# Performance work log

Measured on AMD Instinct MI355X. Metric: run time of the kernel, lower is better.

Reference implementation:

```python
import jax, jax.numpy as jnp
import numpy as np
import math

HEAD_DIM = 32
N_Q_HEADS = 32
N_KV_HEADS = 8
ROPE_BASE = 10000.0
NEG_INF = -1e9


def _rope_cos_sin(seq_len, dtype):
    inv_freq = 1.0 / (ROPE_BASE ** (jnp.arange(0, HEAD_DIM, 2, dtype=jnp.float32) / HEAD_DIM))
    pos = jnp.arange(seq_len, dtype=jnp.float32)
    freqs = pos[:, None] * inv_freq[None, :]          # [S, D/2]
    emb = jnp.concatenate([freqs, freqs], axis=-1)     # [S, D]
    return jnp.cos(emb).astype(dtype), jnp.sin(emb).astype(dtype)


def _rotate_half(x):
    x1, x2 = jnp.split(x, 2, axis=-1)
    return jnp.concatenate([-x2, x1], axis=-1)


def _apply_rope(x, cos, sin):
    # x: [B, H, S, D]; cos/sin: [S, D]
    return x * cos[None, None] + _rotate_half(x) * sin[None, None]


def setup_inputs() -> dict:
    key = jax.random.key(0)
    ks = jax.random.split(key, 5)
    B, S, D = 2, 2048, 1024
    sc = 1.0 / math.sqrt(D)
    return {
        "hidden_states": jax.random.normal(ks[0], (B, S, D), jnp.float32),
        "attention_mask": jnp.ones((B, S), jnp.int32),
        "Wq": jax.random.normal(ks[1], (1024, 1024), jnp.float32) * sc,
        "Wk": jax.random.normal(ks[2], (256, 1024), jnp.float32) * sc,
        "Wv": jax.random.normal(ks[3], (256, 1024), jnp.float32) * sc,
        "Wo": jax.random.normal(ks[4], (1024, 1024), jnp.float32) * sc,
    }


def reference(hidden_states, attention_mask, Wq, Wk, Wv, Wo):
    B, S, D = hidden_states.shape
    group = N_Q_HEADS // N_KV_HEADS

    q = (hidden_states @ Wq.T).reshape(B, S, N_Q_HEADS, HEAD_DIM).transpose(0, 2, 1, 3)
    k = (hidden_states @ Wk.T).reshape(B, S, N_KV_HEADS, HEAD_DIM).transpose(0, 2, 1, 3)
    v = (hidden_states @ Wv.T).reshape(B, S, N_KV_HEADS, HEAD_DIM).transpose(0, 2, 1, 3)

    cos, sin = _rope_cos_sin(S, q.dtype)
    q = _apply_rope(q, cos, sin)
    k = _apply_rope(k, cos, sin)

    k = jnp.repeat(k, group, axis=1)  # [B, 32, S, D]
    v = jnp.repeat(v, group, axis=1)

    scores = jnp.einsum("bhqd,bhkd->bhqk", q, k) / math.sqrt(HEAD_DIM)

    causal = jnp.tril(jnp.ones((S, S), bool))
    allowed = causal[None, None] & (attention_mask[:, None, None, :] != 0)
    scores = jnp.where(allowed, scores, NEG_INF)

    attn = jax.nn.softmax(scores, axis=-1)
    out = jnp.einsum("bhqk,bhkd->bhqd", attn, v)  # [B, 32, S, 32]
    out = out.transpose(0, 2, 1, 3).reshape(B, S, D)
    return out @ Wo.T
```

## Files before the change

### kernel.cpp

```cpp
#include <hip/hip_runtime.h>

typedef __bf16 bf16x8 __attribute__((ext_vector_type(8)));
typedef __bf16 bf16x4 __attribute__((ext_vector_type(4)));
typedef float f32x4 __attribute__((ext_vector_type(4)));

__device__ __forceinline__ f32x4 mfma16(bf16x8 a, bf16x8 b, f32x4 c) {
  return __builtin_amdgcn_mfma_f32_16x16x32_bf16(a, b, c, 0, 0, 0);
}

__device__ __forceinline__ float fast_exp2(float x) {
  return __builtin_amdgcn_exp2f(x);
}

__global__ __launch_bounds__(256) void prep(const float* __restrict__ hidden,
                                            const float* __restrict__ Wq,
                                            const float* __restrict__ Wk,
                                            const float* __restrict__ Wv,
                                            const float* __restrict__ Wo,
                                            __bf16* __restrict__ hb,
                                            __bf16* __restrict__ Wqkvb,
                                            __bf16* __restrict__ Wob) {
  int q = blockIdx.x * 256 + threadIdx.x;
  const float* src;
  __bf16* dst;
  if (q < 1048576) {
    src = hidden; dst = hb;
  } else if ((q -= 1048576) < 262144) {
    src = Wq; dst = Wqkvb;
  } else if ((q -= 262144) < 65536) {
    src = Wk; dst = Wqkvb + 1048576;
  } else if ((q -= 65536) < 65536) {
    src = Wv; dst = Wqkvb + 1310720;
  } else {
    q -= 65536;
    src = Wo; dst = Wob;
  }
  float4 v = *(const float4*)(src + (size_t)q * 4);
  bf16x4 o = { (__bf16)v.x, (__bf16)v.y, (__bf16)v.z, (__bf16)v.w };
  *(bf16x4*)(dst + (size_t)q * 4) = o;
}

template <bool BF16_OUT>
__global__ __launch_bounds__(256) void gemm_nt(const __bf16* __restrict__ A,
                                               const __bf16* __restrict__ B,
                                               void* __restrict__ Cv, int N) {
  __shared__ __bf16 As[2][128][32];
  __shared__ __bf16 Bs[2][128][32];
  const int m0 = blockIdx.x * 128, n0 = blockIdx.y * 128;
  const int tid = threadIdx.x;
  const int wave = tid >> 6, lane = tid & 63, quad = lane >> 4, l16 = lane & 15;
  const int wr = wave >> 1, wc = wave & 1;
  const int sr = tid >> 1, sc = (tid & 1) * 16;
  f32x4 acc[4][4] = {};
  const __bf16* Ap = A + (size_t)(m0 + sr) * 1024 + sc;
  const __bf16* Bp = B + (size_t)(n0 + sr) * 1024 + sc;
  {
    uint4 a0 = *(const uint4*)Ap, a1 = *(const uint4*)(Ap + 8);
    uint4 b0 = *(const uint4*)Bp, b1 = *(const uint4*)(Bp + 8);
    *(uint4*)&As[0][sr][sc] = a0;
    *(uint4*)&As[0][sr][sc + 8] = a1;
    *(uint4*)&Bs[0][sr][sc] = b0;
    *(uint4*)&Bs[0][sr][sc + 8] = b1;
  }
  __syncthreads();
  int buf = 0;
  for (int k0 = 0; k0 < 1024; k0 += 32) {
    const bool more = (k0 + 32) < 1024;
    uint4 na0, na1, nb0, nb1;
    if (more) {
      na0 = *(const uint4*)(Ap + k0 + 32);
      na1 = *(const uint4*)(Ap + k0 + 40);
      nb0 = *(const uint4*)(Bp + k0 + 32);
      nb1 = *(const uint4*)(Bp + k0 + 40);
    }
    bf16x8 af[4], bfr[4];
#pragma unroll
    for (int i = 0; i < 4; i++)
      af[i] = *(bf16x8*)&As[buf][64 * wr + 16 * i + l16][quad * 8];
#pragma unroll
    for (int j = 0; j < 4; j++)
      bfr[j] = *(bf16x8*)&Bs[buf][64 * wc + 16 * j + l16][quad * 8];
#pragma unroll
    for (int i = 0; i < 4; i++)
#pragma unroll
      for (int j = 0; j < 4; j++) acc[i][j] = mfma16(af[i], bfr[j], acc[i][j]);
    if (more) {
      *(uint4*)&As[buf ^ 1][sr][sc] = na0;
      *(uint4*)&As[buf ^ 1][sr][sc + 8] = na1;
      *(uint4*)&Bs[buf ^ 1][sr][sc] = nb0;
      *(uint4*)&Bs[buf ^ 1][sr][sc + 8] = nb1;
    }
    __syncthreads();
    buf ^= 1;
  }
#pragma unroll
  for (int i = 0; i < 4; i++)
#pragma unroll
    for (int j = 0; j < 4; j++)
#pragma unroll
      for (int r = 0; r < 4; r++) {
        int row = m0 + 64 * wr + 16 * i + quad * 4 + r;
        int col = n0 + 64 * wc + 16 * j + l16;
        if constexpr (BF16_OUT)
          ((__bf16*)Cv)[(size_t)row * N + col] = (__bf16)acc[i][j][r];
        else
          ((float*)Cv)[(size_t)row * N + col] = acc[i][j][r];
      }
}

__global__ __launch_bounds__(256) void ropevt(__bf16* __restrict__ QKV,
                                              __bf16* __restrict__ VT,
                                              const int* __restrict__ amask,
                                              float* __restrict__ maskb) {
  int idx = blockIdx.x * 256 + threadIdx.x;
  if (idx < 2621440) {
    __bf16* base;
    int m, i;
    if (idx < 2097152) {
      m = idx >> 9;
      int h = (idx >> 4) & 31;
      i = idx & 15;
      base = QKV + (size_t)m * 1536 + h * 32;
    } else {
      int j = idx - 2097152;
      m = j >> 7;
      int h = (j >> 4) & 7;
      i = j & 15;
      base = QKV + (size_t)m * 1536 + 1024 + h * 32;
    }
    int s = m & 2047;
    float inv = __expf(-(float)i * 0.5756462732485114f);
    float ang = (float)s * inv;
    float sn, cs;
    __sincosf(ang, &sn, &cs);
    float x0 = (float)base[i];
    float x1 = (float)base[i + 16];
    base[i] = (__bf16)(x0 * cs - x1 * sn);
    base[i + 16] = (__bf16)(x1 * cs + x0 * sn);
  } else {
    int j = idx - 2621440;
    if (j < 4096) maskb[j] = amask[j] ? -16.0f : -1.5e9f;
    int s4 = j & 511;
    int d = (j >> 9) & 31;
    int hb_ = j >> 14;
    int s = s4 * 4;
    int b_ = hb_ >> 3, hkv_ = hb_ & 7;
    const __bf16* src = QKV + (size_t)(b_ * 2048 + s) * 1536 + 1280 + hkv_ * 32 + d;
    bf16x4 ov = { src[0], src[1536], src[3072], src[4608] };
    *(bf16x4*)&VT[((size_t)hb_ * 32 + d) * 2048 + s] = ov;
  }
}

__global__ __launch_bounds__(256, 4) void attn(const __bf16* __restrict__ QKV,
                                               const __bf16* __restrict__ VT,
                                               const float* __restrict__ maskb,
                                               __bf16* __restrict__ Ob) {
  __shared__ __bf16 Ks[2][64][40];
  __shared__ __bf16 Vs[2][32][72];
  __shared__ __bf16 Pl[4][2][16][72];
  const int tid = threadIdx.x;
  const int wave = tid >> 6, lane = tid & 63;
  const int quad = lane >> 4, l16 = lane & 15;
  const int b = blockIdx.z, h = blockIdx.y, hkv = h >> 2;
  const int xp = blockIdx.x;
  const float SC2 = 0.25503472f;

  const int sk_key = tid >> 2, sk_ch = (tid & 3) * 8;
  const int sv_d = tid >> 3, sv_seg = (tid & 7) * 8;
  const __bf16* ksrc = QKV + (size_t)(b * 2048 + sk_key) * 1536 + 1024 + hkv * 32 + sk_ch;
  const __bf16* vsrc = VT + ((size_t)(b * 8 + hkv) * 32 + sv_d) * 2048 + sv_seg;
  const float* mrow = maskb + b * 2048;

  for (int sp = 0; sp < 2; sp++) {
    const int strip = sp ? 15 - xp : xp;
    const int qw = strip * 128 + wave * 32;
    const int q_row0 = qw + l16, q_row1 = qw + 16 + l16;
    const __bf16* qbase = QKV + (size_t)(b * 2048 + qw + l16) * 1536 + h * 32 + quad * 8;
    bf16x8 qf0 = *(const bf16x8*)qbase;
    bf16x8 qf1 = *(const bf16x8*)(qbase + 16 * 1536);

    {
      uint4 kr = *(const uint4*)ksrc;
      uint4 vr = *(const uint4*)vsrc;
      *(uint4*)&Ks[0][sk_key][sk_ch] = kr;
      *(uint4*)&Vs[0][sv_d][sv_seg] = vr;
    }
    __syncthreads();

    f32x4 o00 = {}, o01 = {}, o10 = {}, o11 = {};
    float rs0 = 0.f, rs1 = 0.f;
    int buf = 0;
    const int ntiles = 2 * strip + 2;

    for (int t = 0; t < ntiles; t++) {
      const int kv0 = t << 6;
      const bool more = (t + 1 < ntiles);
      uint4 kr, vr;
      if (more) {
        kr = *(const uint4*)(ksrc + (size_t)(t + 1) * 64 * 1536);
        vr = *(const uint4*)(vsrc + (size_t)(t + 1) * 64);
      }
      if (kv0 <= qw + 31) {
        bf16x8 kf[4];
#pragma unroll
        for (int kt = 0; kt < 4; kt++)
          kf[kt] = *(bf16x8*)&Ks[buf][16 * kt + l16][quad * 8];
        f32x4 s0[4], s1[4];
#pragma unroll
        for (int kt = 0; kt < 4; kt++) {
          f32x4 z = {};
          s0[kt] = mfma16(kf[kt], qf0, z);
          s1[kt] = mfma16(kf[kt], qf1, z);
        }
        float p0[4][4], p1[4][4];
        if (kv0 + 63 <= qw) {
#pragma unroll
          for (int kt = 0; kt < 4; kt++) {
            const int kb = kv0 + 16 * kt + 4 * quad;
            float4 mb = *(const float4*)(mrow + kb);
#pragma unroll
            for (int r = 0; r < 4; r++) {
              float e0 = fast_exp2(fmaf(s0[kt][r], SC2, (&mb.x)[r]));
              float e1 = fast_exp2(fmaf(s1[kt][r], SC2, (&mb.x)[r]));
              p0[kt][r] = e0;
              p1[kt][r] = e1;
              rs0 += e0;
              rs1 += e1;
            }
          }
        } else {
#pragma unroll
          for (int kt = 0; kt < 4; kt++) {
            const int kb = kv0 + 16 * kt + 4 * quad;
            float4 mb = *(const float4*)(mrow + kb);
#pragma unroll
            for (int r = 0; r < 4; r++) {
              const int key = kb + r;
              float e0 = fast_exp2(fmaf(s0[kt][r], SC2, (&mb.x)[r]));
              float e1 = fast_exp2(fmaf(s1[kt][r], SC2, (&mb.x)[r]));
              p0[kt][r] = (key <= q_row0) ? e0 : 0.f;
              p1[kt][r] = (key <= q_row1) ? e1 : 0.f;
              rs0 += p0[kt][r];
              rs1 += p1[kt][r];
            }
          }
        }
        bf16x8 vf00 = *(bf16x8*)&Vs[buf][l16][quad * 8];
        bf16x8 vf01 = *(bf16x8*)&Vs[buf][l16][32 + quad * 8];
        bf16x8 vf10 = *(bf16x8*)&Vs[buf][16 + l16][quad * 8];
        bf16x8 vf11 = *(bf16x8*)&Vs[buf][16 + l16][32 + quad * 8];
#pragma unroll
        for (int kt = 0; kt < 4; kt++) {
          bf16x4 pa = { (__bf16)p0[kt][0], (__bf16)p0[kt][1],
                        (__bf16)p0[kt][2], (__bf16)p0[kt][3] };
          bf16x4 pb = { (__bf16)p1[kt][0], (__bf16)p1[kt][1],
                        (__bf16)p1[kt][2], (__bf16)p1[kt][3] };
          *(bf16x4*)&Pl[wave][0][l16][16 * kt + 4 * quad] = pa;
          *(bf16x4*)&Pl[wave][1][l16][16 * kt + 4 * quad] = pb;
        }
        asm volatile("s_waitcnt lgkmcnt(0)" ::: "memory");
        bf16x8 pf00 = *(bf16x8*)&Pl[wave][0][l16][8 * quad];
        bf16x8 pf01 = *(bf16x8*)&Pl[wave][0][l16][32 + 8 * quad];
        bf16x8 pf10 = *(bf16x8*)&Pl[wave][1][l16][8 * quad];
        bf16x8 pf11 = *(bf16x8*)&Pl[wave][1][l16][32 + 8 * quad];
        asm volatile("s_waitcnt lgkmcnt(0)" ::: "memory");
        o00 = mfma16(vf00, pf00, o00);
        o00 = mfma16(vf01, pf01, o00);
        o01 = mfma16(vf10, pf00, o01);
        o01 = mfma16(vf11, pf01, o01);
        o10 = mfma16(vf00, pf10, o10);
        o10 = mfma16(vf01, pf11, o10);
        o11 = mfma16(vf10, pf10, o11);
        o11 = mfma16(vf11, pf11, o11);
      }
      if (more) {
        *(uint4*)&Ks[buf ^ 1][sk_key][sk_ch] = kr;
        *(uint4*)&Vs[buf ^ 1][sv_d][sv_seg] = vr;
      }
      __syncthreads();
      buf ^= 1;
    }
    rs0 += __shfl_xor(rs0, 16);
    rs0 += __shfl_xor(rs0, 32);
    rs1 += __shfl_xor(rs1, 16);
    rs1 += __shfl_xor(rs1, 32);
    float inv0 = 1.0f / rs0, inv1 = 1.0f / rs1;
    size_t row0 = (size_t)(b * 2048 + q_row0);
    size_t row1 = (size_t)(b * 2048 + q_row1);
    bf16x4 w00 = { (__bf16)(o00[0] * inv0), (__bf16)(o00[1] * inv0),
                   (__bf16)(o00[2] * inv0), (__bf16)(o00[3] * inv0) };
    bf16x4 w01 = { (__bf16)(o01[0] * inv0), (__bf16)(o01[1] * inv0),
                   (__bf16)(o01[2] * inv0), (__bf16)(o01[3] * inv0) };
    bf16x4 w10 = { (__bf16)(o10[0] * inv1), (__bf16)(o10[1] * inv1),
                   (__bf16)(o10[2] * inv1), (__bf16)(o10[3] * inv1) };
    bf16x4 w11 = { (__bf16)(o11[0] * inv1), (__bf16)(o11[1] * inv1),
                   (__bf16)(o11[2] * inv1), (__bf16)(o11[3] * inv1) };
    *(bf16x4*)&Ob[row0 * 1024 + h * 32 + quad * 4] = w00;
    *(bf16x4*)&Ob[row0 * 1024 + h * 32 + 16 + quad * 4] = w01;
    *(bf16x4*)&Ob[row1 * 1024 + h * 32 + quad * 4] = w10;
    *(bf16x4*)&Ob[row1 * 1024 + h * 32 + 16 + quad * 4] = w11;
  }
}

extern "C" void kernel_launch(void* const* d_in, const int* in_sizes, int n_in,
                              void* d_out, int out_size, void* d_ws, size_t ws_size,
                              hipStream_t stream) {
  const float* hidden = (const float*)d_in[0];
  const int* amask = (const int*)d_in[1];
  const float* Wq = (const float*)d_in[2];
  const float* Wk = (const float*)d_in[3];
  const float* Wv = (const float*)d_in[4];
  const float* Wo = (const float*)d_in[5];
  float* out = (float*)d_out;

  char* p = (char*)d_ws;
  auto carve = [&](size_t elems) {
    __bf16* r = (__bf16*)p;
    p += ((elems * 2 + 255) / 256) * 256;
    return r;
  };
  __bf16* hb = carve(4096ull * 1024);
  __bf16* Wqkvb = carve(1536ull * 1024);
  __bf16* Wob = carve(1024ull * 1024);
  __bf16* QKV = carve(4096ull * 1536);
  __bf16* VT = carve(4096ull * 256);
  __bf16* Ob = carve(4096ull * 1024);
  float* maskb = (float*)carve(8192);

  prep<<<6656, 256, 0, stream>>>(hidden, Wq, Wk, Wv, Wo, hb, Wqkvb, Wob);

  gemm_nt<true><<<dim3(32, 12), 256, 0, stream>>>(hb, Wqkvb, QKV, 1536);

  ropevt<<<11264, 256, 0, stream>>>(QKV, VT, amask, maskb);

  attn<<<dim3(8, 32, 2), 256, 0, stream>>>(QKV, VT, maskb, Ob);

  gemm_nt<false><<<dim3(32, 8), 256, 0, stream>>>(Ob, Wob, (void*)out, 1024);
}
```

Before: 195.0 us.

## Use direct-to-LDS loads and narrower GEMM tiles; feed P from registers via K16 MFMA

The GEMM kernel now stages A and B tiles with global_load_lds (direct global-to-LDS) instead of going through registers. The N tile shrinks from 128 to 64, which doubles the grid to give more blocks on the many CUs. In attention, the P matrix is kept in registers and fed to 16x16x16 bf16 MFMAs that match the score accumulator layout. This removes the per-wave LDS round trip for P and its waitcnt stalls, and the attention occupancy hint drops from 4 to 2 blocks. The risks are lower arithmetic intensity per GEMM block and twice as many smaller MFMAs in the PV step.

New measurement: 199.7 us. 2.4% more time.

```diff
diff --git a/kernel.cpp b/kernel.cpp
--- a/kernel.cpp
+++ b/kernel.cpp
@@ -2,14 +2,35 @@
 
 typedef __bf16 bf16x8 __attribute__((ext_vector_type(8)));
 typedef __bf16 bf16x4 __attribute__((ext_vector_type(4)));
+typedef short short4v __attribute__((ext_vector_type(4)));
 typedef float f32x4 __attribute__((ext_vector_type(4)));
 
 __device__ __forceinline__ f32x4 mfma16(bf16x8 a, bf16x8 b, f32x4 c) {
   return __builtin_amdgcn_mfma_f32_16x16x32_bf16(a, b, c, 0, 0, 0);
 }
 
+__device__ __forceinline__ f32x4 mfma16k16(bf16x4 a, bf16x4 b, f32x4 c) {
+#if __has_builtin(__builtin_amdgcn_mfma_f32_16x16x16bf16_1k)
+  short4v as = __builtin_bit_cast(short4v, a);
+  short4v bs = __builtin_bit_cast(short4v, b);
+  return __builtin_amdgcn_mfma_f32_16x16x16bf16_1k(as, bs, c, 0, 0, 0);
+#else
+  f32x4 d;
+  asm volatile("v_mfma_f32_16x16x16_bf16 %0, %1, %2, %3"
+               : "=v"(d)
+               : "v"(a), "v"(b), "v"(c));
+  return d;
+#endif
+}
+
 __device__ __forceinline__ float fast_exp2(float x) {
   return __builtin_amdgcn_exp2f(x);
+}
+
+typedef const __attribute__((address_space(1))) void gvoid_t;
+typedef __attribute__((address_space(3))) void svoid_t;
+__device__ __forceinline__ void lds16(const __bf16* g, __bf16* l) {
+  __builtin_amdgcn_global_load_lds((gvoid_t*)g, (svoid_t*)l, 16, 0, 0);
 }
 
 __global__ __launch_bounds__(256) void prep(const float* __restrict__ hidden,
@@ -45,62 +66,48 @@
                                                const __bf16* __restrict__ B,
                                                void* __restrict__ Cv, int N) {
   __shared__ __bf16 As[2][128][32];
-  __shared__ __bf16 Bs[2][128][32];
-  const int m0 = blockIdx.x * 128, n0 = blockIdx.y * 128;
+  __shared__ __bf16 Bs[2][64][32];
+  const int m0 = blockIdx.x * 128, n0 = blockIdx.y * 64;
   const int tid = threadIdx.x;
   const int wave = tid >> 6, lane = tid & 63, quad = lane >> 4, l16 = lane & 15;
   const int wr = wave >> 1, wc = wave & 1;
-  const int sr = tid >> 1, sc = (tid & 1) * 16;
-  f32x4 acc[4][4] = {};
-  const __bf16* Ap = A + (size_t)(m0 + sr) * 1024 + sc;
-  const __bf16* Bp = B + (size_t)(n0 + sr) * 1024 + sc;
-  {
-    uint4 a0 = *(const uint4*)Ap, a1 = *(const uint4*)(Ap + 8);
-    uint4 b0 = *(const uint4*)Bp, b1 = *(const uint4*)(Bp + 8);
-    *(uint4*)&As[0][sr][sc] = a0;
-    *(uint4*)&As[0][sr][sc + 8] = a1;
-    *(uint4*)&Bs[0][sr][sc] = b0;
-    *(uint4*)&Bs[0][sr][sc + 8] = b1;
-  }
+  const int srA = 32 * wave, srB = 16 * wave;
+  const __bf16* Ag = A + (size_t)(m0 + srA + (lane >> 2)) * 1024 + (lane & 3) * 8;
+  const __bf16* Bg = B + (size_t)(n0 + srB + (lane >> 2)) * 1024 + (lane & 3) * 8;
+  f32x4 acc[4][2] = {};
+
+  auto stage = [&](int buf, int k0) {
+    lds16(Ag + k0, &As[buf][srA][0]);
+    lds16(Ag + 16 * 1024 + k0, &As[buf][srA + 16][0]);
+    lds16(Bg + k0, &Bs[buf][srB][0]);
+  };
+  stage(0, 0);
   __syncthreads();
   int buf = 0;
   for (int k0 = 0; k0 < 1024; k0 += 32) {
-    const bool more = (k0 + 32) < 1024;
-    uint4 na0, na1, nb0, nb1;
-    if (more) {
-      na0 = *(const uint4*)(Ap + k0 + 32);
-      na1 = *(const uint4*)(Ap + k0 + 40);
-      nb0 = *(const uint4*)(Bp + k0 + 32);
-      nb1 = *(const uint4*)(Bp + k0 + 40);
-    }
-    bf16x8 af[4], bfr[4];
+    if (k0 + 32 < 1024) stage(buf ^ 1, k0 + 32);
+    bf16x8 af[4], bfr[2];
 #pragma unroll
     for (int i = 0; i < 4; i++)
       af[i] = *(bf16x8*)&As[buf][64 * wr + 16 * i + l16][quad * 8];
 #pragma unroll
-    for (int j = 0; j < 4; j++)
-      bfr[j] = *(bf16x8*)&Bs[buf][64 * wc + 16 * j + l16][quad * 8];
+    for (int j = 0; j < 2; j++)
+      bfr[j] = *(bf16x8*)&Bs[buf][32 * wc + 16 * j + l16][quad * 8];
 #pragma unroll
     for (int i = 0; i < 4; i++)
 #pragma unroll
-      for (int j = 0; j < 4; j++) acc[i][j] = mfma16(af[i], bfr[j], acc[i][j]);
-    if (more) {
-      *(uint4*)&As[buf ^ 1][sr][sc] = na0;
-      *(uint4*)&As[buf ^ 1][sr][sc + 8] = na1;
-      *(uint4*)&Bs[buf ^ 1][sr][sc] = nb0;
-      *(uint4*)&Bs[buf ^ 1][sr][sc + 8] = nb1;
-    }
+      for (int j = 0; j < 2; j++) acc[i][j] = mfma16(af[i], bfr[j], acc[i][j]);
     __syncthreads();
     buf ^= 1;
   }
 #pragma unroll
   for (int i = 0; i < 4; i++)
 #pragma unroll
-    for (int j = 0; j < 4; j++)
+    for (int j = 0; j < 2; j++)
 #pragma unroll
       for (int r = 0; r < 4; r++) {
         int row = m0 + 64 * wr + 16 * i + quad * 4 + r;
-        int col = n0 + 64 * wc + 16 * j + l16;
+        int col = n0 + 32 * wc + 16 * j + l16;
         if constexpr (BF16_OUT)
           ((__bf16*)Cv)[(size_t)row * N + col] = (__bf16)acc[i][j][r];
         else
@@ -151,13 +158,12 @@
   }
 }
 
-__global__ __launch_bounds__(256, 4) void attn(const __bf16* __restrict__ QKV,
+__global__ __launch_bounds__(256, 2) void attn(const __bf16* __restrict__ QKV,
                                                const __bf16* __restrict__ VT,
                                                const float* __restrict__ maskb,
                                                __bf16* __restrict__ Ob) {
   __shared__ __bf16 Ks[2][64][40];
   __shared__ __bf16 Vs[2][32][72];
-  __shared__ __bf16 Pl[4][2][16][72];
   const int tid = threadIdx.x;
   const int wave = tid >> 6, lane = tid & 63;
   const int quad = lane >> 4, l16 = lane & 15;
@@ -212,7 +218,7 @@
           s0[kt] = mfma16(kf[kt], qf0, z);
           s1[kt] = mfma16(kf[kt], qf1, z);
         }
-        float p0[4][4], p1[4][4];
+        bf16x4 pb0[4], pb1[4];
         if (kv0 + 63 <= qw) {
 #pragma unroll
           for (int kt = 0; kt < 4; kt++) {
@@ -222,10 +228,10 @@
             for (int r = 0; r < 4; r++) {
               float e0 = fast_exp2(fmaf(s0[kt][r], SC2, (&mb.x)[r]));
               float e1 = fast_exp2(fmaf(s1[kt][r], SC2, (&mb.x)[r]));
-              p0[kt][r] = e0;
-              p1[kt][r] = e1;
               rs0 += e0;
               rs1 += e1;
+              pb0[kt][r] = (__bf16)e0;
+              pb1[kt][r] = (__bf16)e1;
             }
           }
         } else {
@@ -238,40 +244,24 @@
               const int key = kb + r;
               float e0 = fast_exp2(fmaf(s0[kt][r], SC2, (&mb.x)[r]));
               float e1 = fast_exp2(fmaf(s1[kt][r], SC2, (&mb.x)[r]));
-              p0[kt][r] = (key <= q_row0) ? e0 : 0.f;
-              p1[kt][r] = (key <= q_row1) ? e1 : 0.f;
-              rs0 += p0[kt][r];
-              rs1 += p1[kt][r];
+              e0 = (key <= q_row0) ? e0 : 0.f;
+              e1 = (key <= q_row1) ? e1 : 0.f;
+              rs0 += e0;
+              rs1 += e1;
+              pb0[kt][r] = (__bf16)e0;
+              pb1[kt][r] = (__bf16)e1;
             }
           }
         }
-        bf16x8 vf00 = *(bf16x8*)&Vs[buf][l16][quad * 8];
-        bf16x8 vf01 = *(bf16x8*)&Vs[buf][l16][32 + quad * 8];
-        bf16x8 vf10 = *(bf16x8*)&Vs[buf][16 + l16][quad * 8];
-        bf16x8 vf11 = *(bf16x8*)&Vs[buf][16 + l16][32 + quad * 8];
 #pragma unroll
         for (int kt = 0; kt < 4; kt++) {
-          bf16x4 pa = { (__bf16)p0[kt][0], (__bf16)p0[kt][1],
-                        (__bf16)p0[kt][2], (__bf16)p0[kt][3] };
-          bf16x4 pb = { (__bf16)p1[kt][0], (__bf16)p1[kt][1],
-                        (__bf16)p1[kt][2], (__bf16)p1[kt][3] };
-          *(bf16x4*)&Pl[wave][0][l16][16 * kt + 4 * quad] = pa;
-          *(bf16x4*)&Pl[wave][1][l16][16 * kt + 4 * quad] = pb;
+          bf16x4 v0 = *(bf16x4*)&Vs[buf][l16][16 * kt + 4 * quad];
+          bf16x4 v1 = *(bf16x4*)&Vs[buf][16 + l16][16 * kt + 4 * quad];
+          o00 = mfma16k16(v0, pb0[kt], o00);
+          o01 = mfma16k16(v1, pb0[kt], o01);
+          o10 = mfma16k16(v0, pb1[kt], o10);
+          o11 = mfma16k16(v1, pb1[kt], o11);
         }
-        asm volatile("s_waitcnt lgkmcnt(0)" ::: "memory");
-        bf16x8 pf00 = *(bf16x8*)&Pl[wave][0][l16][8 * quad];
-        bf16x8 pf01 = *(bf16x8*)&Pl[wave][0][l16][32 + 8 * quad];
-        bf16x8 pf10 = *(bf16x8*)&Pl[wave][1][l16][8 * quad];
-        bf16x8 pf11 = *(bf16x8*)&Pl[wave][1][l16][32 + 8 * quad];
-        asm volatile("s_waitcnt lgkmcnt(0)" ::: "memory");
-        o00 = mfma16(vf00, pf00, o00);
-        o00 = mfma16(vf01, pf01, o00);
-        o01 = mfma16(vf10, pf00, o01);
-        o01 = mfma16(vf11, pf01, o01);
-        o10 = mfma16(vf00, pf10, o10);
-        o10 = mfma16(vf01, pf11, o10);
-        o11 = mfma16(vf10, pf10, o11);
-        o11 = mfma16(vf11, pf11, o11);
       }
       if (more) {
         *(uint4*)&Ks[buf ^ 1][sk_key][sk_ch] = kr;
@@ -329,11 +319,11 @@
 
   prep<<<6656, 256, 0, stream>>>(hidden, Wq, Wk, Wv, Wo, hb, Wqkvb, Wob);
 
-  gemm_nt<true><<<dim3(32, 12), 256, 0, stream>>>(hb, Wqkvb, QKV, 1536);
+  gemm_nt<true><<<dim3(32, 24), 256, 0, stream>>>(hb, Wqkvb, QKV, 1536);
 
   ropevt<<<11264, 256, 0, stream>>>(QKV, VT, amask, maskb);
 
   attn<<<dim3(8, 32, 2), 256, 0, stream>>>(QKV, VT, maskb, Ob);
 
-  gemm_nt<false><<<dim3(32, 8), 256, 0, stream>>>(Ob, Wob, (void*)out, 1024);
-}
+  gemm_nt<false><<<dim3(32, 16), 256, 0, stream>>>(Ob, Wob, (void*)out, 1024);
+}
```
